# Kernel tuning notes

Hardware: AMD Instinct MI355X
Metric: run time of the kernel (lower is better)

Reference implementation:

```python
import jax, jax.numpy as jnp
import numpy as np

H, W = 6144, 6144
KH, KW = 3, 3


def setup_inputs() -> dict:
    key = jax.random.key(0)
    k1, k2, k3 = jax.random.split(key, 3)
    x = jax.random.normal(k1, (H, W), dtype=jnp.float32)
    kernel = jax.random.normal(k2, (KH, KW), dtype=jnp.float32)
    bias = jax.random.normal(k3, (1,), dtype=jnp.float32)
    return {"x": x, "kernel": kernel, "bias": bias}


def reference(x, kernel, bias):
    # Valid 2D cross-correlation (no kernel flip), identical math to the
    # per-pixel double loop: out[i,j] = sum(x[i:i+h, j:j+w] * kernel) + bias.
    lhs = x[None, None, :, :]            # [N=1, C=1, H, W]
    rhs = kernel[None, None, :, :]       # [O=1, I=1, h, w]
    out = jax.lax.conv_general_dilated(
        lhs, rhs,
        window_strides=(1, 1),
        padding="VALID",
        dimension_numbers=("NCHW", "OIHW", "NCHW"),
    )[0, 0]                              # [H-h+1, W-w+1]
    return out + bias[0]
```

## Files before the change

### kernel.cpp

```cpp
#include <hip/hip_runtime.h>


#define W_IN  6144
#define H_IN  6144
#define OW    6142
#define OH    6142
#define ROWS  8
#define GRID_X 6
#define GRID_Y 768
#define NWG   (GRID_X * GRID_Y)
#define WG_PER_XCD (NWG / 8)

typedef float f32x2 __attribute__((ext_vector_type(2)));
typedef float f32x4 __attribute__((ext_vector_type(4)));

template <bool INTERIOR>
__device__ __forceinline__ void body_main(const float* __restrict__ x,
                                          float* __restrict__ out,
                                          int c0, int r0,
                                          float k00, float k01, float k02,
                                          float k10, float k11, float k12,
                                          float k20, float k21, float k22,
                                          float bv)
{
    float v[ROWS + 2][6];
#pragma unroll
    for (int r = 0; r < ROWS + 2; ++r) {
        const int rr = r0 + r;
        if (INTERIOR || rr < H_IN) {
            const float* p = x + rr * W_IN + c0;
            const f32x4 a = *reinterpret_cast<const f32x4*>(p);
            const f32x2 c = *reinterpret_cast<const f32x2*>(p + 4);
            v[r][0] = a.x; v[r][1] = a.y; v[r][2] = a.z; v[r][3] = a.w;
            v[r][4] = c.x; v[r][5] = c.y;
        } else {
#pragma unroll
            for (int j = 0; j < 6; ++j) v[r][j] = 0.f;
        }
    }

#pragma unroll
    for (int m = 0; m < ROWS; ++m) {
        const int rr = r0 + m;
        if (INTERIOR || rr < OH) {
            float acc[4];
#pragma unroll
            for (int j = 0; j < 4; ++j) {
                acc[j] = bv
                    + v[m + 0][j] * k00 + v[m + 0][j + 1] * k01 + v[m + 0][j + 2] * k02
                    + v[m + 1][j] * k10 + v[m + 1][j + 1] * k11 + v[m + 1][j + 2] * k12
                    + v[m + 2][j] * k20 + v[m + 2][j + 1] * k21 + v[m + 2][j + 2] * k22;
            }
            float* po = out + rr * OW + c0;
            f32x2 s0; s0.x = acc[0]; s0.y = acc[1];
            f32x2 s1; s1.x = acc[2]; s1.y = acc[3];
            __builtin_nontemporal_store(s0, reinterpret_cast<f32x2*>(po));
            __builtin_nontemporal_store(s1, reinterpret_cast<f32x2*>(po + 2));
        }
    }
}

template <bool INTERIOR>
__device__ __forceinline__ void body_tail(const float* __restrict__ x,
                                          float* __restrict__ out,
                                          int c0, int r0,
                                          float k00, float k01, float k02,
                                          float k10, float k11, float k12,
                                          float k20, float k21, float k22,
                                          float bv)
{
    float v[ROWS + 2][4];
#pragma unroll
    for (int r = 0; r < ROWS + 2; ++r) {
        const int rr = r0 + r;
        if (INTERIOR || rr < H_IN) {
            const f32x4 a = *reinterpret_cast<const f32x4*>(x + rr * W_IN + c0);
            v[r][0] = a.x; v[r][1] = a.y; v[r][2] = a.z; v[r][3] = a.w;
        } else {
#pragma unroll
            for (int j = 0; j < 4; ++j) v[r][j] = 0.f;
        }
    }

#pragma unroll
    for (int m = 0; m < ROWS; ++m) {
        const int rr = r0 + m;
        if (INTERIOR || rr < OH) {
            float a0 = bv
                + v[m + 0][0] * k00 + v[m + 0][1] * k01 + v[m + 0][2] * k02
                + v[m + 1][0] * k10 + v[m + 1][1] * k11 + v[m + 1][2] * k12
                + v[m + 2][0] * k20 + v[m + 2][1] * k21 + v[m + 2][2] * k22;
            float a1 = bv
                + v[m + 0][1] * k00 + v[m + 0][2] * k01 + v[m + 0][3] * k02
                + v[m + 1][1] * k10 + v[m + 1][2] * k11 + v[m + 1][3] * k12
                + v[m + 2][1] * k20 + v[m + 2][2] * k21 + v[m + 2][3] * k22;
            f32x2 s0; s0.x = a0; s0.y = a1;
            __builtin_nontemporal_store(s0, reinterpret_cast<f32x2*>(out + rr * OW + c0));
        }
    }
}

__global__ __launch_bounds__(256)
void corr2d_kernel(const float* __restrict__ x,
                   const float* __restrict__ kk,
                   const float* __restrict__ bias,
                   float* __restrict__ out) {
    const int id = blockIdx.x;
    const int wg = (id & 7) * WG_PER_XCD + (id >> 3);
    const int bx = wg / GRID_Y;
    const int by = wg - bx * GRID_Y;

    const int t  = bx * 256 + (int)threadIdx.x;
    const int c0 = t << 2;
    const int r0 = by * ROWS;

    const float k00 = kk[0], k01 = kk[1], k02 = kk[2];
    const float k10 = kk[3], k11 = kk[4], k12 = kk[5];
    const float k20 = kk[6], k21 = kk[7], k22 = kk[8];
    const float bv = bias[0];

    const bool interior = (r0 + ROWS + 1) < H_IN;

    if (c0 + 4 <= OW) {
        if (interior) body_main<true >(x, out, c0, r0, k00, k01, k02, k10, k11, k12, k20, k21, k22, bv);
        else          body_main<false>(x, out, c0, r0, k00, k01, k02, k10, k11, k12, k20, k21, k22, bv);
    } else {
        if (interior) body_tail<true >(x, out, c0, r0, k00, k01, k02, k10, k11, k12, k20, k21, k22, bv);
        else          body_tail<false>(x, out, c0, r0, k00, k01, k02, k10, k11, k12, k20, k21, k22, bv);
    }
}

extern "C" void kernel_launch(void* const* d_in, const int* in_sizes, int n_in,
                              void* d_out, int out_size, void* d_ws, size_t ws_size,
                              hipStream_t stream) {
    const float* x    = (const float*)d_in[0];
    const float* k    = (const float*)d_in[1];
    const float* bias = (const float*)d_in[2];
    float* out        = (float*)d_out;

    dim3 block(256, 1, 1);
    dim3 grid(NWG, 1, 1);
    corr2d_kernel<<<grid, block, 0, stream>>>(x, k, bias, out);
}
```

Before: 51.12 us.

## Stream tall 48-row bands per thread through an 8-slot register ring buffer

```diff
diff --git a/kernel.cpp b/kernel.cpp
--- a/kernel.cpp
+++ b/kernel.cpp
@@ -5,14 +5,58 @@
 #define H_IN  6144
 #define OW    6142
 #define OH    6142
-#define ROWS  8
+#define BAND  48
+#define NBANDS 128
 #define GRID_X 6
-#define GRID_Y 768
-#define NWG   (GRID_X * GRID_Y)
+#define NWG   (GRID_X * NBANDS)
 #define WG_PER_XCD (NWG / 8)
 
 typedef float f32x2 __attribute__((ext_vector_type(2)));
 typedef float f32x4 __attribute__((ext_vector_type(4)));
+
+
+#define LOAD6(slot, rr)                                                      \
+  {                                                                          \
+    const int rr_ = (rr);                                                    \
+    if (INTERIOR || rr_ < H_IN) {                                            \
+      const float* p_ = x + rr_ * W_IN + c0;                                 \
+      const f32x4 a_ = *reinterpret_cast<const f32x4*>(p_);                  \
+      const f32x2 c_ = *reinterpret_cast<const f32x2*>(p_ + 4);              \
+      v[slot][0] = a_.x; v[slot][1] = a_.y; v[slot][2] = a_.z;               \
+      v[slot][3] = a_.w; v[slot][4] = c_.x; v[slot][5] = c_.y;               \
+    } else {                                                                 \
+      v[slot][0] = 0.f; v[slot][1] = 0.f; v[slot][2] = 0.f;                  \
+      v[slot][3] = 0.f; v[slot][4] = 0.f; v[slot][5] = 0.f;                  \
+    }                                                                        \
+  }
+
+#define STEP6(s, DO_LOAD)                                                    \
+  {                                                                          \
+    if (DO_LOAD) LOAD6(((s) + 7) & 7, rbase + (s) + 7);                      \
+    const int rr = rbase + (s);                                              \
+    if (INTERIOR || rr < OH) {                                               \
+      const float (&ra)[6] = v[(s) & 7];                                     \
+      const float (&rb)[6] = v[((s) + 1) & 7];                               \
+      const float (&rc)[6] = v[((s) + 2) & 7];                               \
+      float acc0 = bv + ra[0]*k00 + ra[1]*k01 + ra[2]*k02                    \
+                      + rb[0]*k10 + rb[1]*k11 + rb[2]*k12                    \
+                      + rc[0]*k20 + rc[1]*k21 + rc[2]*k22;                   \
+      float acc1 = bv + ra[1]*k00 + ra[2]*k01 + ra[3]*k02                    \
+                      + rb[1]*k10 + rb[2]*k11 + rb[3]*k12                    \
+                      + rc[1]*k20 + rc[2]*k21 + rc[3]*k22;                   \
+      float acc2 = bv + ra[2]*k00 + ra[3]*k01 + ra[4]*k02                    \
+                      + rb[2]*k10 + rb[3]*k11 + rb[4]*k12                    \
+                      + rc[2]*k20 + rc[3]*k21 + rc[4]*k22;                   \
+      float acc3 = bv + ra[3]*k00 + ra[4]*k01 + ra[5]*k02                    \
+                      + rb[3]*k10 + rb[4]*k11 + rb[5]*k12                    \
+                      + rc[3]*k20 + rc[4]*k21 + rc[5]*k22;                   \
+      float* po = out + rr * OW + c0;                                        \
+      f32x2 s0_; s0_.x = acc0; s0_.y = acc1;                                 \
+      f32x2 s1_; s1_.x = acc2; s1_.y = acc3;                                 \
+      __builtin_nontemporal_store(s0_, reinterpret_cast<f32x2*>(po));        \
+      __builtin_nontemporal_store(s1_, reinterpret_cast<f32x2*>(po + 2));    \
+    }                                                                        \
+  }
 
 template <bool INTERIOR>
 __device__ __forceinline__ void body_main(const float* __restrict__ x,
@@ -23,42 +67,52 @@
                                           float k20, float k21, float k22,
                                           float bv)
 {
-    float v[ROWS + 2][6];
+    float v[8][6];
 #pragma unroll
-    for (int r = 0; r < ROWS + 2; ++r) {
-        const int rr = r0 + r;
-        if (INTERIOR || rr < H_IN) {
-            const float* p = x + rr * W_IN + c0;
-            const f32x4 a = *reinterpret_cast<const f32x4*>(p);
-            const f32x2 c = *reinterpret_cast<const f32x2*>(p + 4);
-            v[r][0] = a.x; v[r][1] = a.y; v[r][2] = a.z; v[r][3] = a.w;
-            v[r][4] = c.x; v[r][5] = c.y;
-        } else {
-#pragma unroll
-            for (int j = 0; j < 6; ++j) v[r][j] = 0.f;
-        }
+    for (int r = 0; r < 7; ++r) LOAD6(r, r0 + r);
+
+    int rbase = r0;
+    for (int o = 0; o < 5; ++o) {
+        STEP6(0, true) STEP6(1, true) STEP6(2, true) STEP6(3, true)
+        STEP6(4, true) STEP6(5, true) STEP6(6, true) STEP6(7, true)
+        rbase += 8;
     }
+    STEP6(0, true) STEP6(1, true) STEP6(2, true) STEP6(3, false)
+    STEP6(4, false) STEP6(5, false) STEP6(6, false) STEP6(7, false)
+}
 
-#pragma unroll
-    for (int m = 0; m < ROWS; ++m) {
-        const int rr = r0 + m;
-        if (INTERIOR || rr < OH) {
-            float acc[4];
-#pragma unroll
-            for (int j = 0; j < 4; ++j) {
-                acc[j] = bv
-                    + v[m + 0][j] * k00 + v[m + 0][j + 1] * k01 + v[m + 0][j + 2] * k02
-                    + v[m + 1][j] * k10 + v[m + 1][j + 1] * k11 + v[m + 1][j + 2] * k12
-                    + v[m + 2][j] * k20 + v[m + 2][j + 1] * k21 + v[m + 2][j + 2] * k22;
-            }
-            float* po = out + rr * OW + c0;
-            f32x2 s0; s0.x = acc[0]; s0.y = acc[1];
-            f32x2 s1; s1.x = acc[2]; s1.y = acc[3];
-            __builtin_nontemporal_store(s0, reinterpret_cast<f32x2*>(po));
-            __builtin_nontemporal_store(s1, reinterpret_cast<f32x2*>(po + 2));
-        }
-    }
-}
+
+#define LOAD4(slot, rr)                                                      \
+  {                                                                          \
+    const int rr_ = (rr);                                                    \
+    if (INTERIOR || rr_ < H_IN) {                                            \
+      const f32x4 a_ = *reinterpret_cast<const f32x4*>(x + rr_ * W_IN + c0); \
+      v[slot][0] = a_.x; v[slot][1] = a_.y; v[slot][2] = a_.z;               \
+      v[slot][3] = a_.w;                                                     \
+    } else {                                                                 \
+      v[slot][0] = 0.f; v[slot][1] = 0.f; v[slot][2] = 0.f; v[slot][3] = 0.f;\
+    }                                                                        \
+  }
+
+#define STEP4(s, DO_LOAD)                                                    \
+  {                                                                          \
+    if (DO_LOAD) LOAD4(((s) + 7) & 7, rbase + (s) + 7);                      \
+    const int rr = rbase + (s);                                              \
+    if (INTERIOR || rr < OH) {                                               \
+      const float (&ra)[4] = v[(s) & 7];                                     \
+      const float (&rb)[4] = v[((s) + 1) & 7];                               \
+      const float (&rc)[4] = v[((s) + 2) & 7];                               \
+      float a0 = bv + ra[0]*k00 + ra[1]*k01 + ra[2]*k02                      \
+                    + rb[0]*k10 + rb[1]*k11 + rb[2]*k12                      \
+                    + rc[0]*k20 + rc[1]*k21 + rc[2]*k22;                     \
+      float a1 = bv + ra[1]*k00 + ra[2]*k01 + ra[3]*k02                      \
+                    + rb[1]*k10 + rb[2]*k11 + rb[3]*k12                      \
+                    + rc[1]*k20 + rc[2]*k21 + rc[3]*k22;                     \
+      f32x2 s0_; s0_.x = a0; s0_.y = a1;                                     \
+      __builtin_nontemporal_store(s0_,                                       \
+          reinterpret_cast<f32x2*>(out + rr * OW + c0));                     \
+    }                                                                        \
+  }
 
 template <bool INTERIOR>
 __device__ __forceinline__ void body_tail(const float* __restrict__ x,
@@ -69,35 +123,18 @@
                                           float k20, float k21, float k22,
                                           float bv)
 {
-    float v[ROWS + 2][4];
+    float v[8][4];
 #pragma unroll
-    for (int r = 0; r < ROWS + 2; ++r) {
-        const int rr = r0 + r;
-        if (INTERIOR || rr < H_IN) {
-            const f32x4 a = *reinterpret_cast<const f32x4*>(x + rr * W_IN + c0);
-            v[r][0] = a.x; v[r][1] = a.y; v[r][2] = a.z; v[r][3] = a.w;
-        } else {
-#pragma unroll
-            for (int j = 0; j < 4; ++j) v[r][j] = 0.f;
-        }
+    for (int r = 0; r < 7; ++r) LOAD4(r, r0 + r);
+
+    int rbase = r0;
+    for (int o = 0; o < 5; ++o) {
+        STEP4(0, true) STEP4(1, true) STEP4(2, true) STEP4(3, true)
+        STEP4(4, true) STEP4(5, true) STEP4(6, true) STEP4(7, true)
+        rbase += 8;
     }
-
-#pragma unroll
-    for (int m = 0; m < ROWS; ++m) {
-        const int rr = r0 + m;
-        if (INTERIOR || rr < OH) {
-            float a0 = bv
-                + v[m + 0][0] * k00 + v[m + 0][1] * k01 + v[m + 0][2] * k02
-                + v[m + 1][0] * k10 + v[m + 1][1] * k11 + v[m + 1][2] * k12
-                + v[m + 2][0] * k20 + v[m + 2][1] * k21 + v[m + 2][2] * k22;
-            float a1 = bv
-                + v[m + 0][1] * k00 + v[m + 0][2] * k01 + v[m + 0][3] * k02
-                + v[m + 1][1] * k10 + v[m + 1][2] * k11 + v[m + 1][3] * k12
-                + v[m + 2][1] * k20 + v[m + 2][2] * k21 + v[m + 2][3] * k22;
-            f32x2 s0; s0.x = a0; s0.y = a1;
-            __builtin_nontemporal_store(s0, reinterpret_cast<f32x2*>(out + rr * OW + c0));
-        }
-    }
+    STEP4(0, true) STEP4(1, true) STEP4(2, true) STEP4(3, false)
+    STEP4(4, false) STEP4(5, false) STEP4(6, false) STEP4(7, false)
 }
 
 __global__ __launch_bounds__(256)
@@ -107,19 +144,19 @@
                    float* __restrict__ out) {
     const int id = blockIdx.x;
     const int wg = (id & 7) * WG_PER_XCD + (id >> 3);
-    const int bx = wg / GRID_Y;
-    const int by = wg - bx * GRID_Y;
+    const int bx = wg / NBANDS;
+    const int by = wg - bx * NBANDS;
 
     const int t  = bx * 256 + (int)threadIdx.x;
     const int c0 = t << 2;
-    const int r0 = by * ROWS;
+    const int r0 = by * BAND;
 
     const float k00 = kk[0], k01 = kk[1], k02 = kk[2];
     const float k10 = kk[3], k11 = kk[4], k12 = kk[5];
     const float k20 = kk[6], k21 = kk[7], k22 = kk[8];
     const float bv = bias[0];
 
-    const bool interior = (r0 + ROWS + 1) < H_IN;
+    const bool interior = (r0 + BAND + 1) < H_IN;
 
     if (c0 + 4 <= OW) {
         if (interior) body_main<true >(x, out, c0, r0, k00, k01, k02, k10, k11, k12, k20, k21, k22, bv);
```

New measurement: 69.25 us. 35.5% more time.
